# Kernel optimization log

Measured on AMD Instinct MI355X. Metric: run time of the kernel, lower is better.

Reference implementation:

```python
import jax, jax.numpy as jnp
import numpy as np

BETA = 0.1       # reputation weight
GAMMA = 0.1      # load penalty weight
EXPL_C = 0.1     # UCB exploration constant
LOAD_EMA = 0.9   # load EMA alpha
TOP_K = 2
EPS = 1e-10


def setup_inputs() -> dict:
    key = jax.random.key(0)
    k1, k2, k3, k4, k5 = jax.random.split(key, 5)
    B, S, H, E = 4, 4096, 2048, 64
    return {
        "x": jax.random.normal(k1, (B, S, H), dtype=jnp.float32),
        "gate_w": jax.random.normal(k2, (E, H), dtype=jnp.float32) * (1.0 / np.sqrt(H)),
        "reputation": jax.random.normal(k3, (E,), dtype=jnp.float32),
        "loads": jax.random.uniform(k4, (E,), dtype=jnp.float32),
        "counts": jax.random.uniform(k5, (E,), dtype=jnp.float32),
        "total_decisions": 1000000,
    }


def reference(x, gate_w, reputation, loads, counts, total_decisions):
    B, S, H = x.shape
    E = gate_w.shape[0]
    x_flat = x.reshape(-1, H)                                  # [T, H]
    base_logits = jnp.einsum("th,eh->te", x_flat, gate_w)      # [T, E]

    # current_batch_assignments is None -> current_loads = expert_loads
    updated_loads = LOAD_EMA * loads + (1.0 - LOAD_EMA) * loads  # [E]

    # UCB-style exploration bonus, broadcast over tokens
    expl = EXPL_C * jnp.sqrt(jnp.log(jnp.float32(total_decisions) + 1.0) / (counts + EPS))  # [E]

    selection_scores = (base_logits
                        + BETA * reputation[None, :]
                        - GAMMA * updated_loads[None, :]
                        + expl[None, :])                        # [T, E]

    top_k_scores, top_k_indices = jax.lax.top_k(selection_scores, TOP_K)  # [T, K]
    routing_weights = jax.nn.softmax(top_k_scores, axis=-1).reshape(B, S, TOP_K)
    expert_indices = top_k_indices.reshape(B, S, TOP_K)

    # differentiable load-balancing aux loss
    router_probs = jax.nn.softmax(selection_scores.astype(jnp.float32), axis=-1)  # [T, E]
    expert_gate = jax.nn.one_hot(top_k_indices, E, dtype=jnp.float32).sum(axis=1)  # [T, E]
    tokens_per_expert = expert_gate.mean(axis=0)               # [E]
    router_prob_per_expert = router_probs.mean(axis=0)         # [E]
    aux_loss = (tokens_per_expert * router_prob_per_expert).sum() * E

    return routing_weights, expert_indices, aux_loss
```

## Files before the change

### kernel.cpp

```cpp
#include <hip/hip_runtime.h>
#include <cmath>

#define HDIM 2048
#define H4   (HDIM / 4)
#define NEXP 64
#define TTOT 16384
#define BM   64
#define BK   32
#define NITER_FULL (HDIM / BK)
#define KSPLIT 4
#define NITER_K (NITER_FULL / KSPLIT)
#define LDA  (BM + 4)
#define LDB  (NEXP + 4)
#define LDS_SC 65

#define WS_PARTIAL_OFF 128
#define PARTIAL_FLOATS ((size_t)(TTOT / BM) * KSPLIT * BM * NEXP)

__global__ __launch_bounds__(256, 4) void router_gemm_k(
    const float* __restrict__ x,
    const float* __restrict__ gw,
    float* __restrict__ partial)
{
    __shared__ float a_s[2][BK][LDA];
    __shared__ float b_s[2][BK][LDB];

    const int tid = threadIdx.x;
    const int tx  = tid & 15;
    const int ty  = tid >> 4;
    const int r0  = tid >> 3;
    const int c4  = tid & 7;
    const int tb  = blockIdx.x;
    const int kg  = blockIdx.y;
    const int t0  = tb * BM;
    const int kb  = kg * (H4 / KSPLIT);

    const float4* __restrict__ x4 = reinterpret_cast<const float4*>(x) + (size_t)t0 * H4 + kb;
    const float4* __restrict__ g4 = reinterpret_cast<const float4*>(gw) + kb;

    float acc[4][4] = {};

#define STORE_TILE(BUFI, A0, A1, B0, B1) do {                                  \
        float _t0[4] = {(A0).x, (A0).y, (A0).z, (A0).w};                       \
        float _t1[4] = {(A1).x, (A1).y, (A1).z, (A1).w};                       \
        float _t2[4] = {(B0).x, (B0).y, (B0).z, (B0).w};                       \
        float _t3[4] = {(B1).x, (B1).y, (B1).z, (B1).w};                       \
        _Pragma("unroll")                                                      \
        for (int u = 0; u < 4; ++u) {                                          \
            a_s[BUFI][c4 * 4 + u][r0]      = _t0[u];                           \
            a_s[BUFI][c4 * 4 + u][r0 + 32] = _t1[u];                           \
            b_s[BUFI][c4 * 4 + u][r0]      = _t2[u];                           \
            b_s[BUFI][c4 * 4 + u][r0 + 32] = _t3[u];                           \
        } } while (0)

    {
        float4 a0 = x4[(size_t)r0 * H4 + c4];
        float4 a1 = x4[(size_t)(r0 + 32) * H4 + c4];
        float4 b0 = g4[(size_t)r0 * H4 + c4];
        float4 b1 = g4[(size_t)(r0 + 32) * H4 + c4];
        STORE_TILE(0, a0, a1, b0, b1);
    }
    __syncthreads();

    int buf = 0;
    for (int it = 0; it < NITER_K; ++it) {
        float4 na0, na1, nb0, nb1;
        const bool has_next = (it + 1 < NITER_K);
        if (has_next) {
            const int k4 = (it + 1) * (BK / 4);
            na0 = x4[(size_t)r0 * H4 + k4 + c4];
            na1 = x4[(size_t)(r0 + 32) * H4 + k4 + c4];
            nb0 = g4[(size_t)r0 * H4 + k4 + c4];
            nb1 = g4[(size_t)(r0 + 32) * H4 + k4 + c4];
        }

        #pragma unroll
        for (int kk = 0; kk < BK; ++kk) {
            const float4 afv = *reinterpret_cast<const float4*>(&a_s[buf][kk][ty * 4]);
            const float4 bfv = *reinterpret_cast<const float4*>(&b_s[buf][kk][tx * 4]);
            const float af[4] = {afv.x, afv.y, afv.z, afv.w};
            const float bf[4] = {bfv.x, bfv.y, bfv.z, bfv.w};
            #pragma unroll
            for (int i = 0; i < 4; ++i)
                #pragma unroll
                for (int j = 0; j < 4; ++j)
                    acc[i][j] = fmaf(af[i], bf[j], acc[i][j]);
        }

        if (has_next) STORE_TILE(buf ^ 1, na0, na1, nb0, nb1);
        __syncthreads();
        buf ^= 1;
    }
#undef STORE_TILE

    float4* pout = reinterpret_cast<float4*>(partial + ((size_t)tb * KSPLIT + kg) * (BM * NEXP));
    #pragma unroll
    for (int i = 0; i < 4; ++i)
        pout[(ty * 4 + i) * (NEXP / 4) + tx] =
            make_float4(acc[i][0], acc[i][1], acc[i][2], acc[i][3]);
}

__global__ __launch_bounds__(256) void router_reduce(
    const float* __restrict__ partial,
    const float* __restrict__ rep,
    const float* __restrict__ loads,
    const float* __restrict__ counts,
    const int*   __restrict__ total_dec,
    float* __restrict__ out_w,
    float* __restrict__ out_idx,
    float* __restrict__ prob_acc,
    float* __restrict__ gate_acc)
{
    __shared__ float sc_s[BM][LDS_SC];
    __shared__ float bias_s[NEXP];
    __shared__ float m_s[BM], z_s[BM];
    __shared__ int   i1_s[BM], i2_s[BM];

    const int tid = threadIdx.x;
    const int tb  = blockIdx.x;
    const int t0  = tb * BM;

    if (tid < NEXP) {
        float L = logf((float)(*total_dec) + 1.0f);
        bias_s[tid] = 0.1f * rep[tid] - 0.1f * loads[tid]
                    + 0.1f * sqrtf(L / (counts[tid] + 1e-10f));
    }
    __syncthreads();

    const float* p = partial + (size_t)tb * KSPLIT * (BM * NEXP);
    #pragma unroll
    for (int o = 0; o < (BM * NEXP) / 256; ++o) {
        const int idx = o * 256 + tid;
        float s = p[idx] + p[BM * NEXP + idx] + p[2 * BM * NEXP + idx] + p[3 * BM * NEXP + idx];
        sc_s[idx >> 6][idx & 63] = s + bias_s[idx & 63];
    }
    __syncthreads();

    if (tid < BM) {
        const int t = tid;
        float m1 = -INFINITY, m2 = -INFINITY;
        int   i1 = 0, i2 = 0;
        for (int e = 0; e < NEXP; ++e) {
            const float s = sc_s[t][e];
            if (s > m1)      { m2 = m1; i2 = i1; m1 = s; i1 = e; }
            else if (s > m2) { m2 = s; i2 = e; }
        }
        float z = 0.0f;
        for (int e = 0; e < NEXP; ++e) z += expf(sc_s[t][e] - m1);

        const float e2  = expf(m2 - m1);
        const float inv = 1.0f / (1.0f + e2);
        const int   gt  = t0 + t;
        reinterpret_cast<float2*>(out_w)[gt]   = make_float2(inv, e2 * inv);
        reinterpret_cast<float2*>(out_idx)[gt] = make_float2((float)i1, (float)i2);
        m_s[t] = m1; z_s[t] = z; i1_s[t] = i1; i2_s[t] = i2;
    }
    __syncthreads();

    if (tid < NEXP) {
        const int e = tid;
        float ps = 0.0f, gs = 0.0f;
        for (int t = 0; t < BM; ++t) {
            ps += expf(sc_s[t][e] - m_s[t]) / z_s[t];
            gs += (float)((i1_s[t] == e) + (i2_s[t] == e));
        }
        atomicAdd(&prob_acc[e], ps);
        atomicAdd(&gate_acc[e], gs);
    }
}

__global__ __launch_bounds__(256) void router_main(
    const float* __restrict__ x,
    const float* __restrict__ gw,
    const float* __restrict__ rep,
    const float* __restrict__ loads,
    const float* __restrict__ counts,
    const int*   __restrict__ total_dec,
    float* __restrict__ out_w,
    float* __restrict__ out_idx,
    float* __restrict__ prob_acc,
    float* __restrict__ gate_acc)
{
    __shared__ float a_s[2][BK][LDA];
    __shared__ float b_s[2][BK][LDB];
    __shared__ float sc_s[BM][LDS_SC];
    __shared__ float bias_s[NEXP];
    __shared__ float m_s[BM], z_s[BM];
    __shared__ int   i1_s[BM], i2_s[BM];

    const int tid = threadIdx.x;
    const int tx  = tid & 15;
    const int ty  = tid >> 4;
    const int r0  = tid >> 3;
    const int c4  = tid & 7;
    const int t0  = blockIdx.x * BM;

    if (tid < NEXP) {
        float L = logf((float)(*total_dec) + 1.0f);
        bias_s[tid] = 0.1f * rep[tid] - 0.1f * loads[tid]
                    + 0.1f * sqrtf(L / (counts[tid] + 1e-10f));
    }

    const float4* __restrict__ x4 = reinterpret_cast<const float4*>(x) + (size_t)t0 * H4;
    const float4* __restrict__ g4 = reinterpret_cast<const float4*>(gw);

    float acc[4][4] = {};

#define STORE_TILE(BUFI, A0, A1, B0, B1) do {                                  \
        float _t0[4] = {(A0).x, (A0).y, (A0).z, (A0).w};                       \
        float _t1[4] = {(A1).x, (A1).y, (A1).z, (A1).w};                       \
        float _t2[4] = {(B0).x, (B0).y, (B0).z, (B0).w};                       \
        float _t3[4] = {(B1).x, (B1).y, (B1).z, (B1).w};                       \
        _Pragma("unroll")                                                      \
        for (int u = 0; u < 4; ++u) {                                          \
            a_s[BUFI][c4 * 4 + u][r0]      = _t0[u];                           \
            a_s[BUFI][c4 * 4 + u][r0 + 32] = _t1[u];                           \
            b_s[BUFI][c4 * 4 + u][r0]      = _t2[u];                           \
            b_s[BUFI][c4 * 4 + u][r0 + 32] = _t3[u];                           \
        } } while (0)

    {
        float4 a0 = x4[(size_t)r0 * H4 + c4];
        float4 a1 = x4[(size_t)(r0 + 32) * H4 + c4];
        float4 b0 = g4[(size_t)r0 * H4 + c4];
        float4 b1 = g4[(size_t)(r0 + 32) * H4 + c4];
        STORE_TILE(0, a0, a1, b0, b1);
    }
    __syncthreads();

    int buf = 0;
    for (int it = 0; it < NITER_FULL; ++it) {
        float4 na0, na1, nb0, nb1;
        const bool has_next = (it + 1 < NITER_FULL);
        if (has_next) {
            const int k4 = (it + 1) * (BK / 4);
            na0 = x4[(size_t)r0 * H4 + k4 + c4];
            na1 = x4[(size_t)(r0 + 32) * H4 + k4 + c4];
            nb0 = g4[(size_t)r0 * H4 + k4 + c4];
            nb1 = g4[(size_t)(r0 + 32) * H4 + k4 + c4];
        }
        #pragma unroll
        for (int kk = 0; kk < BK; ++kk) {
            const float4 afv = *reinterpret_cast<const float4*>(&a_s[buf][kk][ty * 4]);
            const float4 bfv = *reinterpret_cast<const float4*>(&b_s[buf][kk][tx * 4]);
            const float af[4] = {afv.x, afv.y, afv.z, afv.w};
            const float bf[4] = {bfv.x, bfv.y, bfv.z, bfv.w};
            #pragma unroll
            for (int i = 0; i < 4; ++i)
                #pragma unroll
                for (int j = 0; j < 4; ++j)
                    acc[i][j] = fmaf(af[i], bf[j], acc[i][j]);
        }
        if (has_next) STORE_TILE(buf ^ 1, na0, na1, nb0, nb1);
        __syncthreads();
        buf ^= 1;
    }
#undef STORE_TILE

    #pragma unroll
    for (int i = 0; i < 4; ++i)
        #pragma unroll
        for (int j = 0; j < 4; ++j)
            sc_s[ty * 4 + i][tx * 4 + j] = acc[i][j] + bias_s[tx * 4 + j];
    __syncthreads();

    if (tid < BM) {
        const int t = tid;
        float m1 = -INFINITY, m2 = -INFINITY;
        int   i1 = 0, i2 = 0;
        for (int e = 0; e < NEXP; ++e) {
            const float s = sc_s[t][e];
            if (s > m1)      { m2 = m1; i2 = i1; m1 = s; i1 = e; }
            else if (s > m2) { m2 = s; i2 = e; }
        }
        float z = 0.0f;
        for (int e = 0; e < NEXP; ++e) z += expf(sc_s[t][e] - m1);
        const float e2  = expf(m2 - m1);
        const float inv = 1.0f / (1.0f + e2);
        const int   gt  = t0 + t;
        reinterpret_cast<float2*>(out_w)[gt]   = make_float2(inv, e2 * inv);
        reinterpret_cast<float2*>(out_idx)[gt] = make_float2((float)i1, (float)i2);
        m_s[t] = m1; z_s[t] = z; i1_s[t] = i1; i2_s[t] = i2;
    }
    __syncthreads();

    if (tid < NEXP) {
        const int e = tid;
        float ps = 0.0f, gs = 0.0f;
        for (int t = 0; t < BM; ++t) {
            ps += expf(sc_s[t][e] - m_s[t]) / z_s[t];
            gs += (float)((i1_s[t] == e) + (i2_s[t] == e));
        }
        atomicAdd(&prob_acc[e], ps);
        atomicAdd(&gate_acc[e], gs);
    }
}

__global__ void router_aux(const float* __restrict__ prob_acc,
                           const float* __restrict__ gate_acc,
                           float* __restrict__ out_aux)
{
    const float invT = 1.0f / (float)TTOT;
    const int e = threadIdx.x;
    float v = (gate_acc[e] * invT) * (prob_acc[e] * invT);
    #pragma unroll
    for (int off = 32; off > 0; off >>= 1)
        v += __shfl_down(v, off);
    if (e == 0) out_aux[0] = v * (float)NEXP;
}

extern "C" void kernel_launch(void* const* d_in, const int* in_sizes, int n_in,
                              void* d_out, int out_size, void* d_ws, size_t ws_size,
                              hipStream_t stream)
{
    const float* x      = (const float*)d_in[0];
    const float* gw     = (const float*)d_in[1];
    const float* rep    = (const float*)d_in[2];
    const float* loads  = (const float*)d_in[3];
    const float* counts = (const float*)d_in[4];
    const int*   total  = (const int*)d_in[5];

    float* out     = (float*)d_out;
    float* out_w   = out;
    float* out_idx = out + 32768;
    float* out_aux = out + 65536;

    float* prob_acc = (float*)d_ws;
    float* gate_acc = prob_acc + NEXP;
    float* partial  = (float*)d_ws + WS_PARTIAL_OFF;

    const size_t ws_needed = (WS_PARTIAL_OFF + PARTIAL_FLOATS) * sizeof(float);

    hipMemsetAsync(d_ws, 0, WS_PARTIAL_OFF * sizeof(float), stream);

    if (ws_size >= ws_needed) {
        router_gemm_k<<<dim3(TTOT / BM, KSPLIT), dim3(256), 0, stream>>>(x, gw, partial);
        router_reduce<<<dim3(TTOT / BM), dim3(256), 0, stream>>>(
            partial, rep, loads, counts, total, out_w, out_idx, prob_acc, gate_acc);
    } else {
        router_main<<<dim3(TTOT / BM), dim3(256), 0, stream>>>(
            x, gw, rep, loads, counts, total, out_w, out_idx, prob_acc, gate_acc);
    }
    router_aux<<<dim3(1), dim3(64), 0, stream>>>(prob_acc, gate_acc, out_aux);
}
```

Baseline: 246.0 us.

## Enlarge GEMM tile to 256 tokens with 8x8 microtiles and split-K of 8

The split-K gating GEMM now uses 256-token blocks with an 8x8 register microtile per thread, BK=16, and 8 K-splits instead of 64-token blocks, 4x4 microtiles and 4 splits. Each gate-weight tile is reused across four times as many tokens and the FMA-to-LDS-load ratio rises. In exchange, register pressure grows (64 accumulators, launch bounds lowered to 3 blocks per CU) and the partial buffer doubles, so the reduce kernel reads twice as much data.

```diff
diff --git a/kernel.cpp b/kernel.cpp
--- a/kernel.cpp
+++ b/kernel.cpp
@@ -5,38 +5,222 @@
 #define H4   (HDIM / 4)
 #define NEXP 64
 #define TTOT 16384
-#define BM   64
-#define BK   32
-#define NITER_FULL (HDIM / BK)
-#define KSPLIT 4
-#define NITER_K (NITER_FULL / KSPLIT)
-#define LDA  (BM + 4)
-#define LDB  (NEXP + 4)
+#define KSPLIT 8
+#define KBLK (HDIM / KSPLIT)
+#define BK   16
+#define NTILE (KBLK / BK)
+#define BMB  256
+#define LDA  260
+#define LDB  68
 #define LDS_SC 65
 
 #define WS_PARTIAL_OFF 128
-#define PARTIAL_FLOATS ((size_t)(TTOT / BM) * KSPLIT * BM * NEXP)
-
-__global__ __launch_bounds__(256, 4) void router_gemm_k(
+#define PARTIAL_FLOATS ((size_t)(TTOT / 64) * KSPLIT * 64 * NEXP)
+
+__global__ __launch_bounds__(256, 3) void router_gemm_k(
     const float* __restrict__ x,
     const float* __restrict__ gw,
     float* __restrict__ partial)
 {
     __shared__ float a_s[2][BK][LDA];
     __shared__ float b_s[2][BK][LDB];
+
+    const int tid  = threadIdx.x;
+    const int lane = tid & 63;
+    const int wave = tid >> 6;
+    const int eg   = lane & 7;
+    const int tgl  = lane >> 3;
+    const int tg   = wave * 8 + tgl;
+    const int tb   = blockIdx.x;
+    const int kg   = blockIdx.y;
+    const int T0   = tb * BMB;
+    const int kb4  = kg * (KBLK / 4);
+
+    const int r = tid >> 2;
+    const int c = tid & 3;
+
+    const float4* __restrict__ x4 = reinterpret_cast<const float4*>(x) + (size_t)T0 * H4 + kb4;
+    const float4* __restrict__ g4 = reinterpret_cast<const float4*>(gw) + kb4;
+
+    float acc[8][8] = {};
+
+#define LOAD_TILE(TT, PA, PB) do {                                             \
+        const int _k4 = (TT) * (BK / 4);                                       \
+        _Pragma("unroll")                                                      \
+        for (int j = 0; j < 4; ++j)                                            \
+            PA[j] = x4[(size_t)(r + 64 * j) * H4 + _k4 + c];                   \
+        PB = g4[(size_t)r * H4 + _k4 + c];                                     \
+    } while (0)
+
+#define STORE_TILE(BUFI, PA, PB) do {                                          \
+        _Pragma("unroll")                                                      \
+        for (int j = 0; j < 4; ++j) {                                          \
+            const float _t[4] = {PA[j].x, PA[j].y, PA[j].z, PA[j].w};          \
+            _Pragma("unroll")                                                  \
+            for (int u = 0; u < 4; ++u)                                        \
+                a_s[BUFI][c * 4 + u][r + 64 * j] = _t[u];                      \
+        }                                                                      \
+        const float _t2[4] = {PB.x, PB.y, PB.z, PB.w};                         \
+        _Pragma("unroll")                                                      \
+        for (int u = 0; u < 4; ++u)                                            \
+            b_s[BUFI][c * 4 + u][r] = _t2[u];                                  \
+    } while (0)
+
+    {
+        float4 pa[4]; float4 pb;
+        LOAD_TILE(0, pa, pb);
+        STORE_TILE(0, pa, pb);
+    }
+    __syncthreads();
+
+    int buf = 0;
+    for (int tt = 0; tt < NTILE; ++tt) {
+        float4 na[4]; float4 nb;
+        const bool has_next = (tt + 1 < NTILE);
+        if (has_next) LOAD_TILE(tt + 1, na, nb);
+
+        #pragma unroll
+        for (int kk = 0; kk < BK; ++kk) {
+            const float4 a0 = *reinterpret_cast<const float4*>(&a_s[buf][kk][tg * 8]);
+            const float4 a1 = *reinterpret_cast<const float4*>(&a_s[buf][kk][tg * 8 + 4]);
+            const float4 b0 = *reinterpret_cast<const float4*>(&b_s[buf][kk][eg * 8]);
+            const float4 b1 = *reinterpret_cast<const float4*>(&b_s[buf][kk][eg * 8 + 4]);
+            const float af[8] = {a0.x, a0.y, a0.z, a0.w, a1.x, a1.y, a1.z, a1.w};
+            const float bf[8] = {b0.x, b0.y, b0.z, b0.w, b1.x, b1.y, b1.z, b1.w};
+            #pragma unroll
+            for (int i = 0; i < 8; ++i)
+                #pragma unroll
+                for (int j = 0; j < 8; ++j)
+                    acc[i][j] = fmaf(af[i], bf[j], acc[i][j]);
+        }
+
+        if (has_next) STORE_TILE(buf ^ 1, na, nb);
+        __syncthreads();
+        buf ^= 1;
+    }
+#undef LOAD_TILE
+#undef STORE_TILE
+
+    #pragma unroll
+    for (int i = 0; i < 8; ++i) {
+        const int t_loc = tg * 8 + i;
+        const int rt    = tb * 4 + (t_loc >> 6);
+        const int trow  = t_loc & 63;
+        float4* pout = reinterpret_cast<float4*>(
+            partial + ((size_t)rt * KSPLIT + kg) * (64 * NEXP) + (size_t)trow * NEXP);
+        pout[eg * 2]     = make_float4(acc[i][0], acc[i][1], acc[i][2], acc[i][3]);
+        pout[eg * 2 + 1] = make_float4(acc[i][4], acc[i][5], acc[i][6], acc[i][7]);
+    }
+}
+
+__global__ __launch_bounds__(256) void router_reduce(
+    const float* __restrict__ partial,
+    const float* __restrict__ rep,
+    const float* __restrict__ loads,
+    const float* __restrict__ counts,
+    const int*   __restrict__ total_dec,
+    float* __restrict__ out_w,
+    float* __restrict__ out_idx,
+    float* __restrict__ prob_acc,
+    float* __restrict__ gate_acc)
+{
+    __shared__ float sc_s[64][LDS_SC];
+    __shared__ float bias_s[NEXP];
+    __shared__ float m_s[64], z_s[64];
+    __shared__ int   i1_s[64], i2_s[64];
+
+    const int tid = threadIdx.x;
+    const int rt  = blockIdx.x;
+    const int t0  = rt * 64;
+
+    if (tid < NEXP) {
+        float L = logf((float)(*total_dec) + 1.0f);
+        bias_s[tid] = 0.1f * rep[tid] - 0.1f * loads[tid]
+                    + 0.1f * sqrtf(L / (counts[tid] + 1e-10f));
+    }
+    __syncthreads();
+
+    const float* p = partial + (size_t)rt * KSPLIT * (64 * NEXP);
+    #pragma unroll
+    for (int o = 0; o < (64 * NEXP) / 256; ++o) {
+        const int idx = o * 256 + tid;
+        float s = 0.0f;
+        #pragma unroll
+        for (int g = 0; g < KSPLIT; ++g)
+            s += p[(size_t)g * (64 * NEXP) + idx];
+        sc_s[idx >> 6][idx & 63] = s + bias_s[idx & 63];
+    }
+    __syncthreads();
+
+    if (tid < 64) {
+        const int t = tid;
+        float m1 = -INFINITY, m2 = -INFINITY;
+        int   i1 = 0, i2 = 0;
+        for (int e = 0; e < NEXP; ++e) {
+            const float s = sc_s[t][e];
+            if (s > m1)      { m2 = m1; i2 = i1; m1 = s; i1 = e; }
+            else if (s > m2) { m2 = s; i2 = e; }
+        }
+        float z = 0.0f;
+        for (int e = 0; e < NEXP; ++e) z += expf(sc_s[t][e] - m1);
+
+        const float e2  = expf(m2 - m1);
+        const float inv = 1.0f / (1.0f + e2);
+        const int   gt  = t0 + t;
+        reinterpret_cast<float2*>(out_w)[gt]   = make_float2(inv, e2 * inv);
+        reinterpret_cast<float2*>(out_idx)[gt] = make_float2((float)i1, (float)i2);
+        m_s[t] = m1; z_s[t] = z; i1_s[t] = i1; i2_s[t] = i2;
+    }
+    __syncthreads();
+
+    if (tid < NEXP) {
+        const int e = tid;
+        float ps = 0.0f, gs = 0.0f;
+        for (int t = 0; t < 64; ++t) {
+            ps += expf(sc_s[t][e] - m_s[t]) / z_s[t];
+            gs += (float)((i1_s[t] == e) + (i2_s[t] == e));
+        }
+        atomicAdd(&prob_acc[e], ps);
+        atomicAdd(&gate_acc[e], gs);
+    }
+}
+
+#define BKF  32
+#define LDAF (64 + 4)
+__global__ __launch_bounds__(256) void router_main(
+    const float* __restrict__ x,
+    const float* __restrict__ gw,
+    const float* __restrict__ rep,
+    const float* __restrict__ loads,
+    const float* __restrict__ counts,
+    const int*   __restrict__ total_dec,
+    float* __restrict__ out_w,
+    float* __restrict__ out_idx,
+    float* __restrict__ prob_acc,
+    float* __restrict__ gate_acc)
+{
+    __shared__ float a_s[2][BKF][LDAF];
+    __shared__ float b_s[2][BKF][LDAF];
+    __shared__ float sc_s[64][LDS_SC];
+    __shared__ float bias_s[NEXP];
+    __shared__ float m_s[64], z_s[64];
+    __shared__ int   i1_s[64], i2_s[64];
 
     const int tid = threadIdx.x;
     const int tx  = tid & 15;
     const int ty  = tid >> 4;
     const int r0  = tid >> 3;
     const int c4  = tid & 7;
-    const int tb  = blockIdx.x;
-    const int kg  = blockIdx.y;
-    const int t0  = tb * BM;
-    const int kb  = kg * (H4 / KSPLIT);
-
-    const float4* __restrict__ x4 = reinterpret_cast<const float4*>(x) + (size_t)t0 * H4 + kb;
-    const float4* __restrict__ g4 = reinterpret_cast<const float4*>(gw) + kb;
+    const int t0  = blockIdx.x * 64;
+
+    if (tid < NEXP) {
+        float L = logf((float)(*total_dec) + 1.0f);
+        bias_s[tid] = 0.1f * rep[tid] - 0.1f * loads[tid]
+                    + 0.1f * sqrtf(L / (counts[tid] + 1e-10f));
+    }
+
+    const float4* __restrict__ x4 = reinterpret_cast<const float4*>(x) + (size_t)t0 * H4;
+    const float4* __restrict__ g4 = reinterpret_cast<const float4*>(gw);
 
     float acc[4][4] = {};
 
@@ -63,19 +247,18 @@
     __syncthreads();
 
     int buf = 0;
-    for (int it = 0; it < NITER_K; ++it) {
+    for (int it = 0; it < HDIM / BKF; ++it) {
         float4 na0, na1, nb0, nb1;
-        const bool has_next = (it + 1 < NITER_K);
+        const bool has_next = (it + 1 < HDIM / BKF);
         if (has_next) {
-            const int k4 = (it + 1) * (BK / 4);
+            const int k4 = (it + 1) * (BKF / 4);
             na0 = x4[(size_t)r0 * H4 + k4 + c4];
             na1 = x4[(size_t)(r0 + 32) * H4 + k4 + c4];
             nb0 = g4[(size_t)r0 * H4 + k4 + c4];
             nb1 = g4[(size_t)(r0 + 32) * H4 + k4 + c4];
         }
-
         #pragma unroll
-        for (int kk = 0; kk < BK; ++kk) {
+        for (int kk = 0; kk < BKF; ++kk) {
             const float4 afv = *reinterpret_cast<const float4*>(&a_s[buf][kk][ty * 4]);
             const float4 bfv = *reinterpret_cast<const float4*>(&b_s[buf][kk][tx * 4]);
             const float af[4] = {afv.x, afv.y, afv.z, afv.w};
@@ -86,171 +269,6 @@
                 for (int j = 0; j < 4; ++j)
                     acc[i][j] = fmaf(af[i], bf[j], acc[i][j]);
         }
-
-        if (has_next) STORE_TILE(buf ^ 1, na0, na1, nb0, nb1);
-        __syncthreads();
-        buf ^= 1;
-    }
-#undef STORE_TILE
-
-    float4* pout = reinterpret_cast<float4*>(partial + ((size_t)tb * KSPLIT + kg) * (BM * NEXP));
-    #pragma unroll
-    for (int i = 0; i < 4; ++i)
-        pout[(ty * 4 + i) * (NEXP / 4) + tx] =
-            make_float4(acc[i][0], acc[i][1], acc[i][2], acc[i][3]);
-}
-
-__global__ __launch_bounds__(256) void router_reduce(
-    const float* __restrict__ partial,
-    const float* __restrict__ rep,
-    const float* __restrict__ loads,
-    const float* __restrict__ counts,
-    const int*   __restrict__ total_dec,
-    float* __restrict__ out_w,
-    float* __restrict__ out_idx,
-    float* __restrict__ prob_acc,
-    float* __restrict__ gate_acc)
-{
-    __shared__ float sc_s[BM][LDS_SC];
-    __shared__ float bias_s[NEXP];
-    __shared__ float m_s[BM], z_s[BM];
-    __shared__ int   i1_s[BM], i2_s[BM];
-
-    const int tid = threadIdx.x;
-    const int tb  = blockIdx.x;
-    const int t0  = tb * BM;
-
-    if (tid < NEXP) {
-        float L = logf((float)(*total_dec) + 1.0f);
-        bias_s[tid] = 0.1f * rep[tid] - 0.1f * loads[tid]
-                    + 0.1f * sqrtf(L / (counts[tid] + 1e-10f));
-    }
-    __syncthreads();
-
-    const float* p = partial + (size_t)tb * KSPLIT * (BM * NEXP);
-    #pragma unroll
-    for (int o = 0; o < (BM * NEXP) / 256; ++o) {
-        const int idx = o * 256 + tid;
-        float s = p[idx] + p[BM * NEXP + idx] + p[2 * BM * NEXP + idx] + p[3 * BM * NEXP + idx];
-        sc_s[idx >> 6][idx & 63] = s + bias_s[idx & 63];
-    }
-    __syncthreads();
-
-    if (tid < BM) {
-        const int t = tid;
-        float m1 = -INFINITY, m2 = -INFINITY;
-        int   i1 = 0, i2 = 0;
-        for (int e = 0; e < NEXP; ++e) {
-            const float s = sc_s[t][e];
-            if (s > m1)      { m2 = m1; i2 = i1; m1 = s; i1 = e; }
-            else if (s > m2) { m2 = s; i2 = e; }
-        }
-        float z = 0.0f;
-        for (int e = 0; e < NEXP; ++e) z += expf(sc_s[t][e] - m1);
-
-        const float e2  = expf(m2 - m1);
-        const float inv = 1.0f / (1.0f + e2);
-        const int   gt  = t0 + t;
-        reinterpret_cast<float2*>(out_w)[gt]   = make_float2(inv, e2 * inv);
-        reinterpret_cast<float2*>(out_idx)[gt] = make_float2((float)i1, (float)i2);
-        m_s[t] = m1; z_s[t] = z; i1_s[t] = i1; i2_s[t] = i2;
-    }
-    __syncthreads();
-
-    if (tid < NEXP) {
-        const int e = tid;
-        float ps = 0.0f, gs = 0.0f;
-        for (int t = 0; t < BM; ++t) {
-            ps += expf(sc_s[t][e] - m_s[t]) / z_s[t];
-            gs += (float)((i1_s[t] == e) + (i2_s[t] == e));
-        }
-        atomicAdd(&prob_acc[e], ps);
-        atomicAdd(&gate_acc[e], gs);
-    }
-}
-
-__global__ __launch_bounds__(256) void router_main(
-    const float* __restrict__ x,
-    const float* __restrict__ gw,
-    const float* __restrict__ rep,
-    const float* __restrict__ loads,
-    const float* __restrict__ counts,
-    const int*   __restrict__ total_dec,
-    float* __restrict__ out_w,
-    float* __restrict__ out_idx,
-    float* __restrict__ prob_acc,
-    float* __restrict__ gate_acc)
-{
-    __shared__ float a_s[2][BK][LDA];
-    __shared__ float b_s[2][BK][LDB];
-    __shared__ float sc_s[BM][LDS_SC];
-    __shared__ float bias_s[NEXP];
-    __shared__ float m_s[BM], z_s[BM];
-    __shared__ int   i1_s[BM], i2_s[BM];
-
-    const int tid = threadIdx.x;
-    const int tx  = tid & 15;
-    const int ty  = tid >> 4;
-    const int r0  = tid >> 3;
-    const int c4  = tid & 7;
-    const int t0  = blockIdx.x * BM;
-
-    if (tid < NEXP) {
-        float L = logf((float)(*total_dec) + 1.0f);
-        bias_s[tid] = 0.1f * rep[tid] - 0.1f * loads[tid]
-                    + 0.1f * sqrtf(L / (counts[tid] + 1e-10f));
-    }
-
-    const float4* __restrict__ x4 = reinterpret_cast<const float4*>(x) + (size_t)t0 * H4;
-    const float4* __restrict__ g4 = reinterpret_cast<const float4*>(gw);
-
-    float acc[4][4] = {};
-
-#define STORE_TILE(BUFI, A0, A1, B0, B1) do {                                  \
-        float _t0[4] = {(A0).x, (A0).y, (A0).z, (A0).w};                       \
-        float _t1[4] = {(A1).x, (A1).y, (A1).z, (A1).w};                       \
-        float _t2[4] = {(B0).x, (B0).y, (B0).z, (B0).w};                       \
-        float _t3[4] = {(B1).x, (B1).y, (B1).z, (B1).w};                       \
-        _Pragma("unroll")                                                      \
-        for (int u = 0; u < 4; ++u) {                                          \
-            a_s[BUFI][c4 * 4 + u][r0]      = _t0[u];                           \
-            a_s[BUFI][c4 * 4 + u][r0 + 32] = _t1[u];                           \
-            b_s[BUFI][c4 * 4 + u][r0]      = _t2[u];                           \
-            b_s[BUFI][c4 * 4 + u][r0 + 32] = _t3[u];                           \
-        } } while (0)
-
-    {
-        float4 a0 = x4[(size_t)r0 * H4 + c4];
-        float4 a1 = x4[(size_t)(r0 + 32) * H4 + c4];
-        float4 b0 = g4[(size_t)r0 * H4 + c4];
-        float4 b1 = g4[(size_t)(r0 + 32) * H4 + c4];
-        STORE_TILE(0, a0, a1, b0, b1);
-    }
-    __syncthreads();
-
-    int buf = 0;
-    for (int it = 0; it < NITER_FULL; ++it) {
-        float4 na0, na1, nb0, nb1;
-        const bool has_next = (it + 1 < NITER_FULL);
-        if (has_next) {
-            const int k4 = (it + 1) * (BK / 4);
-            na0 = x4[(size_t)r0 * H4 + k4 + c4];
-            na1 = x4[(size_t)(r0 + 32) * H4 + k4 + c4];
-            nb0 = g4[(size_t)r0 * H4 + k4 + c4];
-            nb1 = g4[(size_t)(r0 + 32) * H4 + k4 + c4];
-        }
-        #pragma unroll
-        for (int kk = 0; kk < BK; ++kk) {
-            const float4 afv = *reinterpret_cast<const float4*>(&a_s[buf][kk][ty * 4]);
-            const float4 bfv = *reinterpret_cast<const float4*>(&b_s[buf][kk][tx * 4]);
-            const float af[4] = {afv.x, afv.y, afv.z, afv.w};
-            const float bf[4] = {bfv.x, bfv.y, bfv.z, bfv.w};
-            #pragma unroll
-            for (int i = 0; i < 4; ++i)
-                #pragma unroll
-                for (int j = 0; j < 4; ++j)
-                    acc[i][j] = fmaf(af[i], bf[j], acc[i][j]);
-        }
         if (has_next) STORE_TILE(buf ^ 1, na0, na1, nb0, nb1);
         __syncthreads();
         buf ^= 1;
@@ -264,7 +282,7 @@
             sc_s[ty * 4 + i][tx * 4 + j] = acc[i][j] + bias_s[tx * 4 + j];
     __syncthreads();
 
-    if (tid < BM) {
+    if (tid < 64) {
         const int t = tid;
         float m1 = -INFINITY, m2 = -INFINITY;
         int   i1 = 0, i2 = 0;
@@ -287,7 +305,7 @@
     if (tid < NEXP) {
         const int e = tid;
         float ps = 0.0f, gs = 0.0f;
-        for (int t = 0; t < BM; ++t) {
+        for (int t = 0; t < 64; ++t) {
             ps += expf(sc_s[t][e] - m_s[t]) / z_s[t];
             gs += (float)((i1_s[t] == e) + (i2_s[t] == e));
         }
@@ -334,11 +352,11 @@
     hipMemsetAsync(d_ws, 0, WS_PARTIAL_OFF * sizeof(float), stream);
 
     if (ws_size >= ws_needed) {
-        router_gemm_k<<<dim3(TTOT / BM, KSPLIT), dim3(256), 0, stream>>>(x, gw, partial);
-        router_reduce<<<dim3(TTOT / BM), dim3(256), 0, stream>>>(
+        router_gemm_k<<<dim3(TTOT / BMB, KSPLIT), dim3(256), 0, stream>>>(x, gw, partial);
+        router_reduce<<<dim3(TTOT / 64), dim3(256), 0, stream>>>(
             partial, rep, loads, counts, total, out_w, out_idx, prob_acc, gate_acc);
     } else {
-        router_main<<<dim3(TTOT / BM), dim3(256), 0, stream>>>(
+        router_main<<<dim3(TTOT / 64), dim3(256), 0, stream>>>(
             x, gw, rep, loads, counts, total, out_w, out_idx, prob_acc, gate_acc);
     }
     router_aux<<<dim3(1), dim3(64), 0, stream>>>(prob_acc, gate_acc, out_aux);
```

Result: slower. 920.6 us (+274.3%).
